# Kernel optimization log

Hardware: AMD Instinct MI355X
Metric: run time of the kernel (lower is better)

## Reference

```python
import jax, jax.numpy as jnp
import numpy as np

DIM = 1024
N_HEADS = 16
HEAD_DIM = DIM // N_HEADS
HIDDEN = int(DIM * 4.0)
EPS = 1e-6


def setup_inputs() -> dict:
    key = jax.random.key(0)
    ks = jax.random.split(key, 12)
    s = 0.02
    return {
        "x": jax.random.normal(ks[0], (32, 577, DIM), dtype=jnp.float32),
        "ln1_g": jnp.ones((DIM,), jnp.float32),
        "ln1_b": jnp.zeros((DIM,), jnp.float32),
        "qkv_w": jax.random.normal(ks[1], (DIM, 3 * DIM), jnp.float32) * s,
        "qkv_b": jnp.zeros((3 * DIM,), jnp.float32),
        "proj_w": jax.random.normal(ks[2], (DIM, DIM), jnp.float32) * s,
        "proj_b": jnp.zeros((DIM,), jnp.float32),
        "ln2_g": jnp.ones((DIM,), jnp.float32),
        "ln2_b": jnp.zeros((DIM,), jnp.float32),
        "fc1_w": jax.random.normal(ks[3], (DIM, HIDDEN), jnp.float32) * s,
        "fc1_b": jnp.zeros((HIDDEN,), jnp.float32),
        "fc2_w": jax.random.normal(ks[4], (HIDDEN, DIM), jnp.float32) * s,
        "fc2_b": jnp.zeros((DIM,), jnp.float32),
    }


def _layernorm(x, g, b):
    mu = jnp.mean(x, axis=-1, keepdims=True)
    var = jnp.mean(jnp.square(x - mu), axis=-1, keepdims=True)
    return (x - mu) * jax.lax.rsqrt(var + EPS) * g + b


def _attention(x, qkv_w, qkv_b, proj_w, proj_b):
    B, T, _ = x.shape
    qkv = x @ qkv_w + qkv_b                               # [B,T,3*DIM]
    qkv = qkv.reshape(B, T, 3, N_HEADS, HEAD_DIM)
    q, k, v = qkv[:, :, 0], qkv[:, :, 1], qkv[:, :, 2]    # [B,T,H,D]
    scale = HEAD_DIM ** -0.5
    scores = jnp.einsum("bqhd,bkhd->bhqk", q, k) * scale  # [B,H,T,T]
    attn = jax.nn.softmax(scores, axis=-1)
    out = jnp.einsum("bhqk,bkhd->bqhd", attn, v).reshape(B, T, DIM)
    return out @ proj_w + proj_b


def reference(x, ln1_g, ln1_b, qkv_w, qkv_b, proj_w, proj_b,
              ln2_g, ln2_b, fc1_w, fc1_b, fc2_w, fc2_b):
    x = x + _attention(_layernorm(x, ln1_g, ln1_b), qkv_w, qkv_b, proj_w, proj_b)
    h = _layernorm(x, ln2_g, ln2_b)
    h = jax.nn.gelu(h @ fc1_w + fc1_b, approximate=False)
    x = x + (h @ fc2_w + fc2_b)
    return x
```

## Files before the change

kernel.cpp:

```cpp
#include <hip/hip_runtime.h>

#define M_TOK 18464
#define TSEQ  577
#define NBATCH 32
#define NH    16
#define HD    64
#define DIMM  1024
#define HIDD  4096
#define NTMK  145

typedef __attribute__((ext_vector_type(4))) float f32x4;
typedef __attribute__((ext_vector_type(8))) short bf8;
typedef __attribute__((ext_vector_type(8))) short s8v;
typedef __attribute__((ext_vector_type(4))) short s4v;

__device__ __forceinline__ short f2bf(float f) {
  union { float f; unsigned u; } c; c.f = f;
  unsigned u = c.u;
  unsigned r = (u + 0x7fffu + ((u >> 16) & 1u)) >> 16;
  return (short)r;
}

__device__ __forceinline__ void gld_lds16(const short* g, short* l) {
  __builtin_amdgcn_global_load_lds(
      (const __attribute__((address_space(1))) unsigned int*)g,
      (__attribute__((address_space(3))) unsigned int*)l, 16, 0, 0);
}

#define MFMA16(a, b, c) __builtin_amdgcn_mfma_f32_16x16x32_bf16(a, b, c, 0, 0, 0)

__global__ __launch_bounds__(256) void conv_t_kernel(const float* __restrict__ W,
                                                     short* __restrict__ WT,
                                                     int K, int N) {
  __shared__ short tile[32][33];
  int bx = blockIdx.x;
  int by = blockIdx.y;
  int t = threadIdx.x;
  int c = t & 31, r = t >> 5;
#pragma unroll
  for (int rr = r; rr < 32; rr += 8)
    tile[rr][c] = f2bf(W[(size_t)(by * 32 + rr) * N + bx * 32 + c]);
  __syncthreads();
#pragma unroll
  for (int rr = r; rr < 32; rr += 8)
    WT[(size_t)(bx * 32 + rr) * K + by * 32 + c] = tile[c][rr];
}

__global__ __launch_bounds__(256) void ln_kernel(const float* __restrict__ x,
                                                 const float* __restrict__ g,
                                                 const float* __restrict__ b,
                                                 short* __restrict__ out) {
  int w = threadIdx.x >> 6, l = threadIdx.x & 63;
  int row = blockIdx.x * 4 + w;
  const float4* xr = (const float4*)(x + (size_t)row * DIMM);
  const float4* g4 = (const float4*)g;
  const float4* b4 = (const float4*)b;
  float4 v[4];
  float s1 = 0.f;
#pragma unroll
  for (int i = 0; i < 4; ++i) {
    v[i] = xr[i * 64 + l];
    s1 += v[i].x + v[i].y + v[i].z + v[i].w;
  }
#pragma unroll
  for (int m = 1; m < 64; m <<= 1) s1 += __shfl_xor(s1, m);
  float mu = s1 * (1.0f / 1024.0f);
  float s2 = 0.f;
#pragma unroll
  for (int i = 0; i < 4; ++i) {
    float dx = v[i].x - mu, dy = v[i].y - mu, dz = v[i].z - mu, dw = v[i].w - mu;
    s2 += dx * dx + dy * dy + dz * dz + dw * dw;
  }
#pragma unroll
  for (int m = 1; m < 64; m <<= 1) s2 += __shfl_xor(s2, m);
  float rs = rsqrtf(s2 * (1.0f / 1024.0f) + 1e-6f);
#pragma unroll
  for (int i = 0; i < 4; ++i) {
    float4 gv = g4[i * 64 + l], bv = b4[i * 64 + l];
    s4v o;
    o[0] = f2bf((v[i].x - mu) * rs * gv.x + bv.x);
    o[1] = f2bf((v[i].y - mu) * rs * gv.y + bv.y);
    o[2] = f2bf((v[i].z - mu) * rs * gv.z + bv.z);
    o[3] = f2bf((v[i].w - mu) * rs * gv.w + bv.w);
    *(s4v*)(out + (size_t)row * DIMM + (i * 64 + l) * 4) = o;
  }
}

template <int EPI>
__global__ __launch_bounds__(256, 4) void gemm_kernel(const short* __restrict__ A,
                                                      const short* __restrict__ BT,
                                                      const float* __restrict__ bias,
                                                      const float* res, short* outh,
                                                      float* outf, int M, int K, int N,
                                                      int lda, int ldb, int ntm, int ntn) {
  __shared__ short lds[16384];
  short* lA = lds;
  short* lB = lds + 8192;
  int grid = ntm * ntn;
  int qd = grid >> 3, rd = grid & 7;
  int x = blockIdx.x & 7, il = blockIdx.x >> 3;
  int gid = x * qd + (x < rd ? x : rd) + il;
  int tnh = ntn >> 1;
  int qa = ntm >> 2, ra = ntm & 3;
  int tm = 0, tn = 0, rem = gid;
#pragma unroll
  for (int rg = 0; rg < 8; ++rg) {
    int i = rg >> 1, j = rg & 1;
    int rows = qa + (i < ra ? 1 : 0);
    int cnt = rows * tnh;
    if (rem < cnt) {
      int rowstart = i * qa + (i < ra ? i : ra);
      tm = rowstart + rem / tnh;
      tn = j * tnh + rem % tnh;
      rem = 0x7fffffff;
    } else if (rem != 0x7fffffff) {
      rem -= cnt;
    }
  }
  int m0 = tm * 128, n0 = tn * 128;
  int t = threadIdx.x, l = t & 63;
  int w = t >> 6, wm = w >> 1, wn = w & 1;
  f32x4 acc[4][4] = {};
  const int NKT = K >> 6;

  for (int it = 0; it < NKT; ++it) {
    __syncthreads();
    int kcol = it << 6;
#pragma unroll
    for (int i = 0; i < 4; i++) {
      int L = i * 256 + t;
      int row = L >> 3, cs = (L & 7) ^ (row & 7);
      int mg = m0 + row;
      if (mg > M - 1) mg = M - 1;
      gld_lds16(A + (size_t)mg * lda + kcol + cs * 8,
                &lA[(i * 256 + (t & 448)) * 8]);
    }
#pragma unroll
    for (int i = 0; i < 4; i++) {
      int L = i * 256 + t;
      int row = L >> 3, cs = (L & 7) ^ (row & 7);
      gld_lds16(BT + (size_t)(n0 + row) * ldb + kcol + cs * 8,
                &lB[(i * 256 + (t & 448)) * 8]);
    }
    __syncthreads();
#pragma unroll
    for (int ks = 0; ks < 2; ++ks) {
      bf8 af[4], bfr[4];
      int g = ks * 4 + (l >> 4);
#pragma unroll
      for (int i = 0; i < 4; i++) {
        int r = wm * 64 + i * 16 + (l & 15);
        af[i] = *(const bf8*)&lA[r * 64 + (g ^ (r & 7)) * 8];
      }
#pragma unroll
      for (int j = 0; j < 4; j++) {
        int r = wn * 64 + j * 16 + (l & 15);
        bfr[j] = *(const bf8*)&lB[r * 64 + (g ^ (r & 7)) * 8];
      }
      __builtin_amdgcn_s_setprio(1);
#pragma unroll
      for (int i = 0; i < 4; i++)
#pragma unroll
        for (int j = 0; j < 4; j++) acc[i][j] = MFMA16(af[i], bfr[j], acc[i][j]);
      __builtin_amdgcn_s_setprio(0);
    }
  }

  if constexpr (EPI == 0 || EPI == 2) {
    __syncthreads();
#pragma unroll
    for (int p = 0; p < 2; ++p) {
      if (wm == p) {
#pragma unroll
        for (int jf = 0; jf < 4; ++jf) {
          int lcol = wn * 64 + jf * 16 + (l & 15);
          float bz = bias[n0 + lcol];
#pragma unroll
          for (int ifr = 0; ifr < 4; ++ifr) {
#pragma unroll
            for (int qv = 0; qv < 4; ++qv) {
              int lrow = ifr * 16 + (l >> 4) * 4 + qv;
              float v = acc[ifr][jf][qv] + bz;
              if constexpr (EPI == 2) v = 0.5f * v * (1.0f + erff(v * 0.70710678118f));
              lds[lrow * 132 + lcol] = f2bf(v);
            }
          }
        }
      }
      __syncthreads();
#pragma unroll
      for (int r2 = 0; r2 < 4; ++r2) {
        int c = r2 * 256 + t;
        int lrow = c >> 4, s8 = c & 15;
        int grow = m0 + p * 64 + lrow;
        s4v lo = *(const s4v*)&lds[lrow * 132 + s8 * 8];
        s4v hi = *(const s4v*)&lds[lrow * 132 + s8 * 8 + 4];
        s8v vv = __builtin_shufflevector(lo, hi, 0, 1, 2, 3, 4, 5, 6, 7);
        if (grow < M)
          __builtin_nontemporal_store(vv, (s8v*)(outh + (size_t)grow * N + n0 + s8 * 8));
      }
      __syncthreads();
    }
  } else {
#pragma unroll
    for (int jf = 0; jf < 4; ++jf) {
      int col = n0 + wn * 64 + jf * 16 + (l & 15);
      float bz = (EPI == 3) ? 0.f : bias[col];
#pragma unroll
      for (int ifr = 0; ifr < 4; ++ifr) {
        int rbase = m0 + wm * 64 + ifr * 16 + (l >> 4) * 4;
#pragma unroll
        for (int qv = 0; qv < 4; ++qv) {
          int row = rbase + qv;
          if (row < M) {
            float v = acc[ifr][jf][qv] + bz;
            size_t idx = (size_t)row * N + col;
            if constexpr (EPI == 1) {
              outf[idx] = v + res[idx];
            } else {
              outf[idx] += v;
            }
          }
        }
      }
    }
  }
}

__global__ __launch_bounds__(256, 4) void attn_kernel(const short* __restrict__ qkv,
                                                      short* __restrict__ aout) {
  __shared__ short lK[64 * 64];
  __shared__ short lV[64 * 64];
  __shared__ short lP[4 * 16 * 64];
  int bid = blockIdx.x;
  int i5 = bid >> 3;
  int bh = ((bid & 7) << 6) + i5 / 5;
  int qt = i5 - (i5 / 5) * 5;
  int b = bh >> 4, h = bh & 15;
  int t = threadIdx.x, w = t >> 6, l = t & 63;
  int m0 = qt * 128;
  const size_t tokbase = (size_t)b * TSEQ;
  unsigned lvb = (unsigned)(uintptr_t)&lV[0];
  const bf8 vones = {0x3F80, 0x3F80, 0x3F80, 0x3F80, 0x3F80, 0x3F80, 0x3F80, 0x3F80};

  bf8 qf[2][2];
#pragma unroll
  for (int g = 0; g < 2; ++g) {
    int tq0 = m0 + w * 32 + g * 16 + (l & 15);
    if (tq0 > TSEQ - 1) tq0 = TSEQ - 1;
    const short* qrow = qkv + (tokbase + tq0) * 3072 + h * 64;
    qf[g][0] = *(const bf8*)(qrow + (l >> 4) * 8);
    qf[g][1] = *(const bf8*)(qrow + 32 + (l >> 4) * 8);
  }

  f32x4 o_acc[2][4] = {};
  f32x4 l_acc[2] = {};

  for (int kt = 0; kt < 10; ++kt) {
    __syncthreads();
#pragma unroll
    for (int i = 0; i < 2; i++) {
      int L = i * 256 + t;
      int key = L >> 3;
      int cd = (L & 7) ^ (key & 7);
      int tok = kt * 64 + key; if (tok > TSEQ - 1) tok = TSEQ - 1;
      gld_lds16(qkv + (tokbase + tok) * 3072 + 1024 + h * 64 + cd * 8,
                &lK[(i * 256 + w * 64) * 8]);
    }
#pragma unroll
    for (int i = 0; i < 2; i++) {
      int L = i * 256 + t;
      int k = (L >> 5) * 4 + ((L >> 1) & 3);
      int c = ((L >> 3) & 3) * 2 + (L & 1);
      int tok = kt * 64 + k; if (tok > TSEQ - 1) tok = TSEQ - 1;
      gld_lds16(qkv + (tokbase + tok) * 3072 + 2048 + h * 64 + c * 8,
                &lV[(i * 256 + w * 64) * 8]);
    }
    __syncthreads();

#pragma unroll
    for (int g = 0; g < 2; ++g) {
      __builtin_amdgcn_s_setprio(1);
#pragma unroll
      for (int nf = 0; nf < 4; ++nf) {
        f32x4 a = {};
#pragma unroll
        for (int ks = 0; ks < 2; ++ks) {
          int keyrow = nf * 16 + (l & 15);
          int cp = (ks * 4 + (l >> 4)) ^ (keyrow & 7);
          bf8 kf = *(const bf8*)&lK[keyrow * 64 + cp * 8];
          a = MFMA16(kf, qf[g][ks], a);
        }
        float s0 = a[0] * 0.18033688011f, s1 = a[1] * 0.18033688011f;
        float s2 = a[2] * 0.18033688011f, s3 = a[3] * 0.18033688011f;
        if (kt == 9) {
          int kb = 576 + nf * 16 + 4 * (l >> 4);
          if (kb + 0 >= TSEQ) s0 = -1e30f;
          if (kb + 1 >= TSEQ) s1 = -1e30f;
          if (kb + 2 >= TSEQ) s2 = -1e30f;
          if (kb + 3 >= TSEQ) s3 = -1e30f;
        }
        float e0, e1, e2, e3;
        asm("v_exp_f32 %0, %1" : "=v"(e0) : "v"(s0));
        asm("v_exp_f32 %0, %1" : "=v"(e1) : "v"(s1));
        asm("v_exp_f32 %0, %1" : "=v"(e2) : "v"(s2));
        asm("v_exp_f32 %0, %1" : "=v"(e3) : "v"(s3));
        unsigned d0, d1;
        asm("v_cvt_pk_bf16_f32 %0, %1, %2" : "=v"(d0) : "v"(e0), "v"(e1));
        asm("v_cvt_pk_bf16_f32 %0, %1, %2" : "=v"(d1) : "v"(e2), "v"(e3));
        int row = l & 15;
        int chunk = 2 * nf + ((l >> 4) >> 1);
        int cs = chunk ^ (row & 7);
        int base = w * 1024 + row * 64 + cs * 8 + 4 * ((l >> 4) & 1);
        *(unsigned*)&lP[base] = d0;
        *(unsigned*)&lP[base + 2] = d1;
      }
      __builtin_amdgcn_s_setprio(0);
      asm volatile("s_waitcnt lgkmcnt(0)" ::: "memory");
      __builtin_amdgcn_sched_barrier(0);

#pragma unroll
      for (int ks = 0; ks < 2; ++ks) {
        int qr = l & 15;
        int cp = (ks * 4 + (l >> 4)) ^ (qr & 7);
        bf8 pf = *(const bf8*)&lP[w * 1024 + qr * 64 + cp * 8];
        unsigned kq0 = (unsigned)(ks * 8 + (l >> 4) * 2);
        unsigned abase = lvb + kq0 * 512u + (unsigned)(l & 15) * 8u;
        s4v ra0, ra1, rb0, rb1, rc0, rc1, rd0, rd1;
        asm volatile("ds_read_b64_tr_b16 %0, %1" : "=v"(ra0) : "v"(abase));
        asm volatile("ds_read_b64_tr_b16 %0, %1" : "=v"(ra1) : "v"(abase + 512u));
        asm volatile("ds_read_b64_tr_b16 %0, %1" : "=v"(rb0) : "v"(abase + 128u));
        asm volatile("ds_read_b64_tr_b16 %0, %1" : "=v"(rb1) : "v"(abase + 640u));
        asm volatile("ds_read_b64_tr_b16 %0, %1" : "=v"(rc0) : "v"(abase + 256u));
        asm volatile("ds_read_b64_tr_b16 %0, %1" : "=v"(rc1) : "v"(abase + 768u));
        asm volatile("ds_read_b64_tr_b16 %0, %1" : "=v"(rd0) : "v"(abase + 384u));
        asm volatile("ds_read_b64_tr_b16 %0, %1" : "=v"(rd1) : "v"(abase + 896u));
        asm volatile("s_waitcnt lgkmcnt(0)" ::: "memory");
        __builtin_amdgcn_sched_barrier(0);
        bf8 vfa = __builtin_shufflevector(ra0, ra1, 0, 1, 2, 3, 4, 5, 6, 7);
        bf8 vfb = __builtin_shufflevector(rb0, rb1, 0, 1, 2, 3, 4, 5, 6, 7);
        bf8 vfc = __builtin_shufflevector(rc0, rc1, 0, 1, 2, 3, 4, 5, 6, 7);
        bf8 vfd = __builtin_shufflevector(rd0, rd1, 0, 1, 2, 3, 4, 5, 6, 7);
        __builtin_amdgcn_s_setprio(1);
        l_acc[g] = MFMA16(pf, vones, l_acc[g]);
        o_acc[g][0] = MFMA16(pf, vfa, o_acc[g][0]);
        o_acc[g][1] = MFMA16(pf, vfb, o_acc[g][1]);
        o_acc[g][2] = MFMA16(pf, vfc, o_acc[g][2]);
        o_acc[g][3] = MFMA16(pf, vfd, o_acc[g][3]);
        __builtin_amdgcn_s_setprio(0);
      }
    }
  }
#pragma unroll
  for (int g = 0; g < 2; ++g)
#pragma unroll
    for (int df = 0; df < 4; df++)
#pragma unroll
      for (int q = 0; q < 4; q++) {
        int tq = m0 + w * 32 + g * 16 + (l >> 4) * 4 + q;
        if (tq < TSEQ) {
          float val = o_acc[g][df][q] / l_acc[g][q];
          aout[(tokbase + tq) * DIMM + h * 64 + df * 16 + (l & 15)] = f2bf(val);
        }
      }
}

extern "C" void kernel_launch(void* const* d_in, const int* in_sizes, int n_in,
                              void* d_out, int out_size, void* d_ws, size_t ws_size,
                              hipStream_t stream) {
  const float* x      = (const float*)d_in[0];
  const float* ln1_g  = (const float*)d_in[1];
  const float* ln1_b  = (const float*)d_in[2];
  const float* qkv_w  = (const float*)d_in[3];
  const float* qkv_b  = (const float*)d_in[4];
  const float* proj_w = (const float*)d_in[5];
  const float* proj_b = (const float*)d_in[6];
  const float* ln2_g  = (const float*)d_in[7];
  const float* ln2_b  = (const float*)d_in[8];
  const float* fc1_w  = (const float*)d_in[9];
  const float* fc1_b  = (const float*)d_in[10];
  const float* fc2_w  = (const float*)d_in[11];
  const float* fc2_b  = (const float*)d_in[12];
  float* out = (float*)d_out;

  const size_t REQ = (size_t)(12582912 + (size_t)M_TOK * 1024 + (size_t)M_TOK * 3072) * 2;
  if (ws_size < REQ) return;

  short* w_qkv  = (short*)d_ws;
  short* w_proj = w_qkv + (size_t)3072 * 1024;
  short* w_fc1  = w_proj + (size_t)1024 * 1024;
  short* w_fc2  = w_fc1 + (size_t)4096 * 1024;
  short* bufA   = w_fc2 + (size_t)1024 * 4096;
  short* bufB   = bufA + (size_t)M_TOK * 1024;

  dim3 blk(256);
  conv_t_kernel<<<dim3(3072 / 32, 1024 / 32), blk, 0, stream>>>(qkv_w, w_qkv, 1024, 3072);
  conv_t_kernel<<<dim3(1024 / 32, 1024 / 32), blk, 0, stream>>>(proj_w, w_proj, 1024, 1024);
  conv_t_kernel<<<dim3(4096 / 32, 1024 / 32), blk, 0, stream>>>(fc1_w, w_fc1, 1024, 4096);
  conv_t_kernel<<<dim3(1024 / 32, 4096 / 32), blk, 0, stream>>>(fc2_w, w_fc2, 4096, 1024);
  ln_kernel<<<M_TOK / 4, blk, 0, stream>>>(x, ln1_g, ln1_b, bufA);
  gemm_kernel<0><<<NTMK * 24, blk, 0, stream>>>(bufA, w_qkv, qkv_b, nullptr, bufB, nullptr,
                                                M_TOK, 1024, 3072, 1024, 1024, NTMK, 24);
  attn_kernel<<<2560, blk, 0, stream>>>(bufB, bufA);
  gemm_kernel<1><<<NTMK * 8, blk, 0, stream>>>(bufA, w_proj, proj_b, x, nullptr, out,
                                               M_TOK, 1024, 1024, 1024, 1024, NTMK, 8);
  ln_kernel<<<M_TOK / 4, blk, 0, stream>>>(out, ln2_g, ln2_b, bufA);
  for (int c = 0; c < 2; ++c) {
    gemm_kernel<2><<<NTMK * 16, blk, 0, stream>>>(bufA, w_fc1 + (size_t)c * 2048 * 1024,
                                                  fc1_b + c * 2048, nullptr, bufB, nullptr,
                                                  M_TOK, 1024, 2048, 1024, 1024, NTMK, 16);
    if (c == 0) {
      gemm_kernel<1><<<NTMK * 8, blk, 0, stream>>>(bufB, w_fc2 + (size_t)c * 2048, fc2_b,
                                                   out, nullptr, out, M_TOK, 2048, 1024,
                                                   2048, 4096, NTMK, 8);
    } else {
      gemm_kernel<3><<<NTMK * 8, blk, 0, stream>>>(bufB, w_fc2 + (size_t)c * 2048, fc2_b,
                                                   out, nullptr, out, M_TOK, 2048, 1024,
                                                   2048, 4096, NTMK, 8);
    }
  }
}
```

Baseline: 924.1 us.

## Replace 128x128 GEMM with 256x256 tile, 512-thread, double-buffered pipelined kernel

The GEMM kernel now computes 256x256 output tiles with 8 waves and a 128 KB LDS footprint holding two K-stages of A and B. Global-to-LDS loads for the next stages are issued in quarter steps interleaved with the MFMA work, using explicit vmcnt waits and barriers in place of the old load-then-compute loop with full syncs. The larger tile raises arithmetic intensity and cuts redundant operand traffic. In exchange it drops to one block per CU and wastes more work on the partial last M tile (73 tiles of 256 for 18464 rows).

Result: slower. 1.147 ms (+24.1%).

```diff
diff --git a/kernel.cpp b/kernel.cpp
--- a/kernel.cpp
+++ b/kernel.cpp
@@ -7,7 +7,7 @@
 #define HD    64
 #define DIMM  1024
 #define HIDD  4096
-#define NTMK  145
+#define NTM2  73
 
 typedef __attribute__((ext_vector_type(4))) float f32x4;
 typedef __attribute__((ext_vector_type(8))) short bf8;
@@ -87,15 +87,13 @@
 }
 
 template <int EPI>
-__global__ __launch_bounds__(256, 4) void gemm_kernel(const short* __restrict__ A,
-                                                      const short* __restrict__ BT,
-                                                      const float* __restrict__ bias,
-                                                      const float* res, short* outh,
-                                                      float* outf, int M, int K, int N,
-                                                      int lda, int ldb, int ntm, int ntn) {
-  __shared__ short lds[16384];
-  short* lA = lds;
-  short* lB = lds + 8192;
+__global__ __launch_bounds__(512, 1) void gemm256_kernel(const short* __restrict__ A,
+                                                         const short* __restrict__ BT,
+                                                         const float* __restrict__ bias,
+                                                         const float* res, short* outh,
+                                                         float* outf, int M, int K, int N,
+                                                         int lda, int ldb, int ntm, int ntn) {
+  __shared__ short lds[65536];
   int grid = ntm * ntn;
   int qd = grid >> 3, rd = grid & 7;
   int x = blockIdx.x & 7, il = blockIdx.x >> 3;
@@ -117,87 +115,130 @@
       rem -= cnt;
     }
   }
-  int m0 = tm * 128, n0 = tn * 128;
+  int m0 = tm * 256, n0 = tn * 256;
   int t = threadIdx.x, l = t & 63;
-  int w = t >> 6, wm = w >> 1, wn = w & 1;
-  f32x4 acc[4][4] = {};
+  int w = t >> 6, wm = w >> 2, wn = w & 3;
+  f32x4 acc[8][4] = {};
   const int NKT = K >> 6;
-
-  for (int it = 0; it < NKT; ++it) {
-    __syncthreads();
-    int kcol = it << 6;
-#pragma unroll
-    for (int i = 0; i < 4; i++) {
-      int L = i * 256 + t;
-      int row = L >> 3, cs = (L & 7) ^ (row & 7);
-      int mg = m0 + row;
-      if (mg > M - 1) mg = M - 1;
-      gld_lds16(A + (size_t)mg * lda + kcol + cs * 8,
-                &lA[(i * 256 + (t & 448)) * 8]);
-    }
-#pragma unroll
-    for (int i = 0; i < 4; i++) {
-      int L = i * 256 + t;
-      int row = L >> 3, cs = (L & 7) ^ (row & 7);
-      gld_lds16(BT + (size_t)(n0 + row) * ldb + kcol + cs * 8,
-                &lB[(i * 256 + (t & 448)) * 8]);
-    }
-    __syncthreads();
-#pragma unroll
-    for (int ks = 0; ks < 2; ++ks) {
-      bf8 af[4], bfr[4];
-      int g = ks * 4 + (l >> 4);
-#pragma unroll
-      for (int i = 0; i < 4; i++) {
-        int r = wm * 64 + i * 16 + (l & 15);
-        af[i] = *(const bf8*)&lA[r * 64 + (g ^ (r & 7)) * 8];
-      }
-#pragma unroll
-      for (int j = 0; j < 4; j++) {
-        int r = wn * 64 + j * 16 + (l & 15);
-        bfr[j] = *(const bf8*)&lB[r * 64 + (g ^ (r & 7)) * 8];
-      }
-      __builtin_amdgcn_s_setprio(1);
-#pragma unroll
-      for (int i = 0; i < 4; i++)
-#pragma unroll
-        for (int j = 0; j < 4; j++) acc[i][j] = MFMA16(af[i], bfr[j], acc[i][j]);
-      __builtin_amdgcn_s_setprio(0);
+  const int NIT = NKT >> 1;
+
+  auto STAGE = [&](const short* G, int rbase, int rmax, int ld, int kt, int half, int base) {
+    int kcol = kt << 6;
+#pragma unroll
+    for (int j = 0; j < 2; ++j) {
+      int c = j * 512 + t;
+      int row = c >> 3, cs = (c & 7) ^ (row & 7);
+      int gr = rbase + half * 128 + row;
+      if (gr > rmax) gr = rmax;
+      gld_lds16(G + (size_t)gr * ld + kcol + cs * 8,
+                &lds[base + half * 8192 + (j * 512 + (t & 448)) * 8]);
+    }
+  };
+
+  STAGE(BT, n0, N - 1, ldb, 0, 0, 16384);
+  STAGE(BT, n0, N - 1, ldb, 0, 1, 16384);
+  STAGE(A, m0, M - 1, lda, 0, 0, 0);
+  STAGE(A, m0, M - 1, lda, 0, 1, 0);
+  STAGE(BT, n0, N - 1, ldb, 1, 0, 49152);
+  STAGE(BT, n0, N - 1, ldb, 1, 1, 49152);
+  asm volatile("s_waitcnt vmcnt(4)" ::: "memory");
+  __builtin_amdgcn_s_barrier();
+  __builtin_amdgcn_sched_barrier(0);
+
+  for (int it = 0; it < NIT; ++it) {
+    int t0 = 2 * it, t1 = 2 * it + 1;
+    bool more = (it < NIT - 1);
+#pragma unroll
+    for (int hk = 0; hk < 2; ++hk) {
+      int aB = hk ? 32768 : 0, bB = hk ? 49152 : 16384;
+      bf8 bfr[4][2], af[2][2];
+#pragma unroll
+      for (int q = 0; q < 4; ++q) {
+        if (q == 0) {
+#pragma unroll
+          for (int nf = 0; nf < 4; ++nf)
+#pragma unroll
+            for (int ks = 0; ks < 2; ++ks) {
+              int rB = wn * 64 + nf * 16 + (l & 15);
+              int g = ks * 4 + (l >> 4);
+              bfr[nf][ks] = *(const bf8*)&lds[bB + (rB >> 7) * 8192 + (rB & 127) * 64 +
+                                              ((g ^ (rB & 7)) * 8)];
+            }
+        }
+#pragma unroll
+        for (int i2 = 0; i2 < 2; ++i2)
+#pragma unroll
+          for (int ks = 0; ks < 2; ++ks) {
+            int r = wm * 128 + q * 32 + i2 * 16 + (l & 15);
+            int g = ks * 4 + (l >> 4);
+            af[i2][ks] = *(const bf8*)&lds[aB + (r >> 7) * 8192 + (r & 127) * 64 +
+                                           ((g ^ (r & 7)) * 8)];
+          }
+        if (hk == 0) {
+          if (q == 0)      STAGE(A, m0, M - 1, lda, t1, 0, 32768);
+          else if (q == 1) STAGE(A, m0, M - 1, lda, t1, 1, 32768);
+          else if (q == 2) { if (more) STAGE(BT, n0, N - 1, ldb, t0 + 2, 0, 16384); }
+          else             { if (more) STAGE(BT, n0, N - 1, ldb, t0 + 2, 1, 16384); }
+        } else {
+          if (q == 0)      { if (more) STAGE(A, m0, M - 1, lda, t0 + 2, 0, 0); }
+          else if (q == 1) { if (more) STAGE(A, m0, M - 1, lda, t0 + 2, 1, 0); }
+          else if (q == 2) { if (more) STAGE(BT, n0, N - 1, ldb, t1 + 2, 0, 49152); }
+          else             { if (more) STAGE(BT, n0, N - 1, ldb, t1 + 2, 1, 49152); }
+        }
+        __builtin_amdgcn_s_barrier();
+        asm volatile("s_waitcnt lgkmcnt(0)" ::: "memory");
+        __builtin_amdgcn_sched_barrier(0);
+        __builtin_amdgcn_s_setprio(1);
+#pragma unroll
+        for (int i2 = 0; i2 < 2; ++i2)
+#pragma unroll
+          for (int nf = 0; nf < 4; ++nf)
+#pragma unroll
+            for (int ks = 0; ks < 2; ++ks)
+              acc[q * 2 + i2][nf] = MFMA16(af[i2][ks], bfr[nf][ks], acc[q * 2 + i2][nf]);
+        __builtin_amdgcn_s_setprio(0);
+        if (q == 3) {
+          if (more) asm volatile("s_waitcnt vmcnt(4)" ::: "memory");
+          else      asm volatile("s_waitcnt vmcnt(0)" ::: "memory");
+        }
+        __builtin_amdgcn_s_barrier();
+        __builtin_amdgcn_sched_barrier(0);
+      }
     }
   }
 
   if constexpr (EPI == 0 || EPI == 2) {
-    __syncthreads();
-#pragma unroll
-    for (int p = 0; p < 2; ++p) {
-      if (wm == p) {
+#pragma unroll
+    for (int rg = 0; rg < 4; ++rg) {
+      if (wm == (rg >> 1)) {
+        int i0 = (rg & 1) * 4;
 #pragma unroll
         for (int jf = 0; jf < 4; ++jf) {
           int lcol = wn * 64 + jf * 16 + (l & 15);
           float bz = bias[n0 + lcol];
 #pragma unroll
-          for (int ifr = 0; ifr < 4; ++ifr) {
+          for (int ii = 0; ii < 4; ++ii) {
 #pragma unroll
             for (int qv = 0; qv < 4; ++qv) {
-              int lrow = ifr * 16 + (l >> 4) * 4 + qv;
-              float v = acc[ifr][jf][qv] + bz;
+              int lrow = ii * 16 + (l >> 4) * 4 + qv;
+              float v = acc[i0 + ii][jf][qv] + bz;
               if constexpr (EPI == 2) v = 0.5f * v * (1.0f + erff(v * 0.70710678118f));
-              lds[lrow * 132 + lcol] = f2bf(v);
+              lds[lrow * 264 + lcol] = f2bf(v);
             }
           }
         }
       }
       __syncthreads();
 #pragma unroll
-      for (int r2 = 0; r2 < 4; ++r2) {
-        int c = r2 * 256 + t;
-        int lrow = c >> 4, s8 = c & 15;
-        int grow = m0 + p * 64 + lrow;
-        s4v lo = *(const s4v*)&lds[lrow * 132 + s8 * 8];
-        s4v hi = *(const s4v*)&lds[lrow * 132 + s8 * 8 + 4];
+      for (int it2 = 0; it2 < 4; ++it2) {
+        int c = it2 * 512 + t;
+        int lrow = c >> 5, ch = c & 31;
+        int grow = m0 + rg * 64 + lrow;
+        s4v lo = *(const s4v*)&lds[lrow * 264 + ch * 8];
+        s4v hi = *(const s4v*)&lds[lrow * 264 + ch * 8 + 4];
         s8v vv = __builtin_shufflevector(lo, hi, 0, 1, 2, 3, 4, 5, 6, 7);
         if (grow < M)
-          __builtin_nontemporal_store(vv, (s8v*)(outh + (size_t)grow * N + n0 + s8 * 8));
+          __builtin_nontemporal_store(vv, (s8v*)(outh + (size_t)grow * N + n0 + ch * 8));
       }
       __syncthreads();
     }
@@ -207,8 +248,8 @@
       int col = n0 + wn * 64 + jf * 16 + (l & 15);
       float bz = (EPI == 3) ? 0.f : bias[col];
 #pragma unroll
-      for (int ifr = 0; ifr < 4; ++ifr) {
-        int rbase = m0 + wm * 64 + ifr * 16 + (l >> 4) * 4;
+      for (int ifr = 0; ifr < 8; ++ifr) {
+        int rbase = m0 + wm * 128 + ifr * 16 + (l >> 4) * 4;
 #pragma unroll
         for (int qv = 0; qv < 4; ++qv) {
           int row = rbase + qv;
@@ -394,29 +435,31 @@
   short* bufB   = bufA + (size_t)M_TOK * 1024;
 
   dim3 blk(256);
+  dim3 blk512(512);
   conv_t_kernel<<<dim3(3072 / 32, 1024 / 32), blk, 0, stream>>>(qkv_w, w_qkv, 1024, 3072);
   conv_t_kernel<<<dim3(1024 / 32, 1024 / 32), blk, 0, stream>>>(proj_w, w_proj, 1024, 1024);
   conv_t_kernel<<<dim3(4096 / 32, 1024 / 32), blk, 0, stream>>>(fc1_w, w_fc1, 1024, 4096);
   conv_t_kernel<<<dim3(1024 / 32, 4096 / 32), blk, 0, stream>>>(fc2_w, w_fc2, 4096, 1024);
   ln_kernel<<<M_TOK / 4, blk, 0, stream>>>(x, ln1_g, ln1_b, bufA);
-  gemm_kernel<0><<<NTMK * 24, blk, 0, stream>>>(bufA, w_qkv, qkv_b, nullptr, bufB, nullptr,
-                                                M_TOK, 1024, 3072, 1024, 1024, NTMK, 24);
+  gemm256_kernel<0><<<NTM2 * 12, blk512, 0, stream>>>(bufA, w_qkv, qkv_b, nullptr, bufB,
+                                                      nullptr, M_TOK, 1024, 3072, 1024, 1024,
+                                                      NTM2, 12);
   attn_kernel<<<2560, blk, 0, stream>>>(bufB, bufA);
-  gemm_kernel<1><<<NTMK * 8, blk, 0, stream>>>(bufA, w_proj, proj_b, x, nullptr, out,
-                                               M_TOK, 1024, 1024, 1024, 1024, NTMK, 8);
+  gemm256_kernel<1><<<NTM2 * 4, blk512, 0, stream>>>(bufA, w_proj, proj_b, x, nullptr, out,
+                                                     M_TOK, 1024, 1024, 1024, 1024, NTM2, 4);
   ln_kernel<<<M_TOK / 4, blk, 0, stream>>>(out, ln2_g, ln2_b, bufA);
   for (int c = 0; c < 2; ++c) {
-    gemm_kernel<2><<<NTMK * 16, blk, 0, stream>>>(bufA, w_fc1 + (size_t)c * 2048 * 1024,
-                                                  fc1_b + c * 2048, nullptr, bufB, nullptr,
-                                                  M_TOK, 1024, 2048, 1024, 1024, NTMK, 16);
+    gemm256_kernel<2><<<NTM2 * 8, blk512, 0, stream>>>(bufA, w_fc1 + (size_t)c * 2048 * 1024,
+                                                       fc1_b + c * 2048, nullptr, bufB, nullptr,
+                                                       M_TOK, 1024, 2048, 1024, 1024, NTM2, 8);
     if (c == 0) {
-      gemm_kernel<1><<<NTMK * 8, blk, 0, stream>>>(bufB, w_fc2 + (size_t)c * 2048, fc2_b,
-                                                   out, nullptr, out, M_TOK, 2048, 1024,
-                                                   2048, 4096, NTMK, 8);
+      gemm256_kernel<1><<<NTM2 * 4, blk512, 0, stream>>>(bufB, w_fc2 + (size_t)c * 2048, fc2_b,
+                                                         out, nullptr, out, M_TOK, 2048, 1024,
+                                                         2048, 4096, NTM2, 4);
     } else {
-      gemm_kernel<3><<<NTMK * 8, blk, 0, stream>>>(bufB, w_fc2 + (size_t)c * 2048, fc2_b,
-                                                   out, nullptr, out, M_TOK, 2048, 1024,
-                                                   2048, 4096, NTMK, 8);
-    }
-  }
-}
+      gemm256_kernel<3><<<NTM2 * 4, blk512, 0, stream>>>(bufB, w_fc2 + (size_t)c * 2048, fc2_b,
+                                                         out, nullptr, out, M_TOK, 2048, 1024,
+                                                         2048, 4096, NTM2, 4);
+    }
+  }
+}
```
